# Kernel tuning notes

Hardware: AMD Instinct MI355X
Metric: run time of the kernel (lower is better)

The kernel has to match this reference:

```python
import jax, jax.numpy as jnp
import numpy as np

HEADS = 16


def _linear(x, w, b):
    # torch nn.Linear: y = x @ W^T + b, W: (out, in)
    return jnp.einsum('bld,od->blo', x, w) + b


def setup_inputs() -> dict:
    key = jax.random.key(0)
    ks = jax.random.split(key, 11)
    B, L, QD, KVD = 8, 2048, 1024, 1024
    s_in = 1.0 / np.sqrt(QD)
    return {
        'query': jax.random.normal(ks[0], (B, L, QD), jnp.float32),
        'key':   jax.random.normal(ks[1], (B, L, KVD), jnp.float32),
        'value': jax.random.normal(ks[2], (B, L, KVD), jnp.float32),
        'wq_w': jax.random.normal(ks[3], (KVD, QD), jnp.float32) * s_in,
        'wq_b': jnp.zeros((KVD,), jnp.float32),
        'wk_w': jax.random.normal(ks[4], (KVD, KVD), jnp.float32) * s_in,
        'wk_b': jnp.zeros((KVD,), jnp.float32),
        'wv_w': jax.random.normal(ks[5], (KVD, KVD), jnp.float32) * s_in,
        'wv_b': jnp.zeros((KVD,), jnp.float32),
        'fo_w': jax.random.normal(ks[6], (QD, KVD), jnp.float32) * s_in,
        'fo_b': jnp.zeros((QD,), jnp.float32),
    }


def reference(query, key, value, wq_w, wq_b, wk_w, wk_b, wv_w, wv_b, fo_w, fo_b):
    B, Lq, _ = query.shape
    Lk = key.shape[1]
    kvd = wq_w.shape[0]
    head_dim = kvd // HEADS
    # reshape WITHOUT transpose, exactly as the torch source: (B, L, heads, head_dim)
    q = _linear(query, wq_w, wq_b).reshape(B, Lq, HEADS, head_dim)
    k = _linear(key,   wk_w, wk_b).reshape(B, Lk, HEADS, head_dim)
    v = _linear(value, wv_w, wv_b).reshape(B, Lk, HEADS, head_dim)
    scale = 1.0 / jnp.sqrt(jnp.float32(head_dim))
    # Faithful to source: seq axis acts as 'h'; heads axis is contracted (i,j).
    scores = jnp.einsum('bhid,bhjd->bhij', q, k) * scale  # (B, L, heads, heads)
    weights = jax.nn.softmax(scores, axis=-1)
    out = jnp.einsum('bhij,bhjd->bhid', weights, v)       # (B, L, heads, head_dim)
    out = out.reshape(B, Lq, kvd)
    return _linear(out, fo_w, fo_b)
```

## Files before the change

### kernel.cpp

```cpp
#include <hip/hip_runtime.h>
#include <hip/hip_bf16.h>


typedef __attribute__((ext_vector_type(8))) __bf16 bf16x8;
typedef __attribute__((ext_vector_type(4))) float f32x4;

#define BM 128
#define BN 128
#define BK 64

__device__ __forceinline__ float bf2f(ushort u) {
  union { unsigned int i; float f; } c; c.i = ((unsigned int)u) << 16; return c.f;
}
__device__ __forceinline__ ushort f2b(float f) {
  union { float f; unsigned int i; } c; c.f = f;
  unsigned int x = c.i;
  return (ushort)((x + 0x7FFFu + ((x >> 16) & 1u)) >> 16);
}

__global__ __launch_bounds__(256)
void cvt_f32_bf16(const float* __restrict__ s, ushort* __restrict__ d, int n8)
{
  int i = blockIdx.x * 256 + threadIdx.x;
  if (i >= n8) return;
  const float4* sp = reinterpret_cast<const float4*>(s) + (size_t)i * 2;
  float4 a = sp[0], b = sp[1];
  ushort u[8] = { f2b(a.x), f2b(a.y), f2b(a.z), f2b(a.w),
                  f2b(b.x), f2b(b.y), f2b(b.z), f2b(b.w) };
  reinterpret_cast<uint4*>(d)[i] = *reinterpret_cast<uint4*>(u);
}

__global__ __launch_bounds__(256)
void cvt_wo_perm(const float* __restrict__ w, ushort* __restrict__ o)
{
  int t = blockIdx.x * 256 + threadIdx.x;
  int n  = t >> 7;
  int i8 = (t & 127) << 3;
  int blk = i8 >> 8, g = (i8 >> 6) & 3, i = (i8 >> 2) & 15;
  const float* src = w + (size_t)n * 1024;
  int c = blk * 16 + g * 4;
  float4 a = *reinterpret_cast<const float4*>(src + i * 64 + c);
  float4 b = *reinterpret_cast<const float4*>(src + (i + 1) * 64 + c);
  ushort u[8] = { f2b(a.x), f2b(a.y), f2b(a.z), f2b(a.w),
                  f2b(b.x), f2b(b.y), f2b(b.z), f2b(b.w) };
  *reinterpret_cast<uint4*>(o + (size_t)n * 1024 + i8) = *reinterpret_cast<uint4*>(u);
}

template<int CMODE>
__global__ __launch_bounds__(512, 2)
void gemm8p(const ushort* __restrict__ A, const ushort* __restrict__ Bw,
            const float* __restrict__ bias, void* __restrict__ Cv,
            int M, int N, int K)
{
  extern __shared__ ushort lds[];

  const int tid  = threadIdx.x;
  const int lane = tid & 63;
  const int wid  = tid >> 6;
  const int wm   = wid >> 2;
  const int wn   = wid & 3;

  const int nwg = gridDim.x * gridDim.y;
  int fid = blockIdx.y * gridDim.x + blockIdx.x;
  if ((nwg & 7) == 0) fid = (fid & 7) * (nwg >> 3) + (fid >> 3);
  const int bx = fid % gridDim.x;
  const int by = fid / gridDim.x;
  const int m0 = by * 256, n0 = bx * 256;

  const int NT = K >> 6;

  const int csw = ((lane & 7) ^ (lane >> 3)) << 3;
  auto STAGE = [&](int h, int kt, int b) {
    const ushort* base = (h >= 2) ? Bw : A;
    const int o0 = (h >= 2) ? n0 : m0;
    const int rl = (h & 1) * 128;
    #pragma unroll
    for (int j = 0; j < 2; ++j) {
      int rt = rl + j * 64 + wid * 8;
      const ushort* src = base + (size_t)(o0 + rt + (lane >> 3)) * K + kt * 64 + csw;
      ushort* dst = lds + b * 32768 + (h >= 2 ? 16384 : 0) + rt * 64;
      __builtin_amdgcn_global_load_lds(
          (const __attribute__((address_space(1))) void*)src,
          (__attribute__((address_space(3))) void*)dst, 16, 0, 0);
    }
  };

  auto LDA = [&](int b, int mi, int kk) -> bf16x8 {
    int row  = (mi & 3) * 16 + wm * 64 + (mi >> 2) * 128 + (lane & 15);
    int slot = kk * 4 + (lane >> 4);
    int byte = row * 128 + (((slot ^ (row & 7)) & 7) << 4);
    return *reinterpret_cast<const bf16x8*>((const char*)(lds + b * 32768) + byte);
  };
  auto LDB = [&](int b, int ni, int kk) -> bf16x8 {
    int row  = (ni & 1) * 16 + wn * 32 + (ni >> 1) * 128 + (lane & 15);
    int slot = kk * 4 + (lane >> 4);
    int byte = row * 128 + (((slot ^ (row & 7)) & 7) << 4);
    return *reinterpret_cast<const bf16x8*>((const char*)(lds + b * 32768 + 16384) + byte);
  };

  f32x4 acc[8][4] = {};
  bf16x8 af[4][2], bf[4][2];

  STAGE(0, 0, 0); STAGE(2, 0, 0); STAGE(3, 0, 0); STAGE(1, 0, 0);
  asm volatile("s_waitcnt vmcnt(4)" ::: "memory");
  __builtin_amdgcn_s_barrier();

  for (int t = 0; t < NT; ++t) {
    const int cur = t & 1;
    const int nxt = cur ^ 1;
    const bool pf = (t + 1) < NT;

    #pragma unroll
    for (int i = 0; i < 4; ++i) { af[i][0] = LDA(cur, i, 0); af[i][1] = LDA(cur, i, 1); }
    #pragma unroll
    for (int n = 0; n < 2; ++n) { bf[n][0] = LDB(cur, n, 0); bf[n][1] = LDB(cur, n, 1); }
    if (pf) { STAGE(0, t + 1, nxt); asm volatile("s_waitcnt vmcnt(4)" ::: "memory"); }
    else    {                       asm volatile("s_waitcnt vmcnt(2)" ::: "memory"); }
    __builtin_amdgcn_s_barrier();
    asm volatile("s_waitcnt lgkmcnt(0)" ::: "memory");
    __builtin_amdgcn_sched_barrier(0);
    __builtin_amdgcn_s_setprio(1);
    #pragma unroll
    for (int i = 0; i < 4; ++i)
      #pragma unroll
      for (int n = 0; n < 2; ++n)
        #pragma unroll
        for (int kk = 0; kk < 2; ++kk)
          acc[i][n] = __builtin_amdgcn_mfma_f32_16x16x32_bf16(af[i][kk], bf[n][kk], acc[i][n], 0, 0, 0);
    __builtin_amdgcn_s_setprio(0);
    __builtin_amdgcn_s_barrier();

    #pragma unroll
    for (int n = 0; n < 2; ++n) { bf[2 + n][0] = LDB(cur, 2 + n, 0); bf[2 + n][1] = LDB(cur, 2 + n, 1); }
    if (pf) { STAGE(2, t + 1, nxt); asm volatile("s_waitcnt vmcnt(4)" ::: "memory"); }
    else    {                       asm volatile("s_waitcnt vmcnt(0)" ::: "memory"); }
    __builtin_amdgcn_s_barrier();
    asm volatile("s_waitcnt lgkmcnt(0)" ::: "memory");
    __builtin_amdgcn_sched_barrier(0);
    __builtin_amdgcn_s_setprio(1);
    #pragma unroll
    for (int i = 0; i < 4; ++i)
      #pragma unroll
      for (int n = 0; n < 2; ++n)
        #pragma unroll
        for (int kk = 0; kk < 2; ++kk)
          acc[i][2 + n] = __builtin_amdgcn_mfma_f32_16x16x32_bf16(af[i][kk], bf[2 + n][kk], acc[i][2 + n], 0, 0, 0);
    __builtin_amdgcn_s_setprio(0);
    __builtin_amdgcn_s_barrier();

    #pragma unroll
    for (int i = 0; i < 4; ++i) { af[i][0] = LDA(cur, 4 + i, 0); af[i][1] = LDA(cur, 4 + i, 1); }
    if (pf) STAGE(3, t + 1, nxt);
    __builtin_amdgcn_s_barrier();
    asm volatile("s_waitcnt lgkmcnt(0)" ::: "memory");
    __builtin_amdgcn_sched_barrier(0);
    __builtin_amdgcn_s_setprio(1);
    #pragma unroll
    for (int i = 0; i < 4; ++i)
      #pragma unroll
      for (int n = 0; n < 2; ++n)
        #pragma unroll
        for (int kk = 0; kk < 2; ++kk)
          acc[4 + i][n] = __builtin_amdgcn_mfma_f32_16x16x32_bf16(af[i][kk], bf[n][kk], acc[4 + i][n], 0, 0, 0);
    __builtin_amdgcn_s_setprio(0);
    __builtin_amdgcn_s_barrier();

    if (pf) { STAGE(1, t + 1, nxt); asm volatile("s_waitcnt vmcnt(4)" ::: "memory"); }
    __builtin_amdgcn_s_barrier();
    __builtin_amdgcn_s_setprio(1);
    #pragma unroll
    for (int i = 0; i < 4; ++i)
      #pragma unroll
      for (int n = 0; n < 2; ++n)
        #pragma unroll
        for (int kk = 0; kk < 2; ++kk)
          acc[4 + i][2 + n] = __builtin_amdgcn_mfma_f32_16x16x32_bf16(af[i][kk], bf[2 + n][kk], acc[4 + i][2 + n], 0, 0, 0);
    __builtin_amdgcn_s_setprio(0);
    __builtin_amdgcn_s_barrier();
  }

  #pragma unroll
  for (int ni = 0; ni < 4; ++ni) {
    int col = n0 + (ni & 1) * 16 + wn * 32 + (ni >> 1) * 128 + (lane & 15);
    float bv = bias[col];
    #pragma unroll
    for (int mi = 0; mi < 8; ++mi) {
      int row0 = m0 + (mi & 3) * 16 + wm * 64 + (mi >> 2) * 128 + ((lane >> 4) << 2);
      #pragma unroll
      for (int q = 0; q < 4; ++q) {
        float v = acc[mi][ni][q] + bv;
        if constexpr (CMODE == 0)
          ((float*)Cv)[(size_t)(row0 + q) * N + col] = v;
        else if constexpr (CMODE == 1)
          ((ushort*)Cv)[(size_t)(row0 + q) * N + col] = f2b(v);
        else
          ((ushort*)Cv)[(size_t)(row0 + q) * N + ((col & 63) << 4) + (col >> 6)] = f2b(v);
      }
    }
  }
}

__global__ __launch_bounds__(256)
void attn_mfma(const ushort* __restrict__ Q, const ushort* __restrict__ Kh,
               const ushort* __restrict__ Vt, ushort* __restrict__ Ot, int P)
{
  const int lane = threadIdx.x & 63;
  const int wid  = threadIdx.x >> 6;
  const int g = lane >> 4, c = lane & 15;
  const int stride = gridDim.x * 4;

  for (int p = blockIdx.x * 4 + wid; p < P; p += stride) {
    const ushort* qb = Q  + (size_t)p * 1024;
    const ushort* kb = Kh + (size_t)p * 1024;
    const ushort* vb = Vt + (size_t)p * 1024;

    bf16x8 qf0 = *reinterpret_cast<const bf16x8*>(qb + c * 64 + g * 8);
    bf16x8 qf1 = *reinterpret_cast<const bf16x8*>(qb + c * 64 + 32 + g * 8);
    bf16x8 kf0 = *reinterpret_cast<const bf16x8*>(kb + c * 64 + g * 8);
    bf16x8 kf1 = *reinterpret_cast<const bf16x8*>(kb + c * 64 + 32 + g * 8);

    f32x4 s = {};
    s = __builtin_amdgcn_mfma_f32_16x16x32_bf16(kf0, qf0, s, 0, 0, 0);
    s = __builtin_amdgcn_mfma_f32_16x16x32_bf16(kf1, qf1, s, 0, 0, 0);

    float s0 = s[0] * 0.125f, s1 = s[1] * 0.125f;
    float s2 = s[2] * 0.125f, s3 = s[3] * 0.125f;
    float m = fmaxf(fmaxf(s0, s1), fmaxf(s2, s3));
    m = fmaxf(m, __shfl_xor(m, 16));
    m = fmaxf(m, __shfl_xor(m, 32));
    float e0 = __expf(s0 - m), e1 = __expf(s1 - m);
    float e2 = __expf(s2 - m), e3 = __expf(s3 - m);
    float sum = e0 + e1 + e2 + e3;
    sum += __shfl_xor(sum, 16);
    sum += __shfl_xor(sum, 32);
    float r = 1.0f / sum;

    uint pk0 = (uint)f2b(e0 * r) | ((uint)f2b(e1 * r) << 16);
    uint pk1 = (uint)f2b(e2 * r) | ((uint)f2b(e3 * r) << 16);
    int src = ((g & 1) << 5) | c;
    uint y0 = (uint)__shfl((int)pk0, src);
    uint y1 = (uint)__shfl((int)pk1, src);
    uint y2 = (uint)__shfl((int)pk0, src | 16);
    uint y3 = (uint)__shfl((int)pk1, src | 16);
    if (g >= 2) { y0 = 0; y1 = 0; y2 = 0; y3 = 0; }
    union { uint u[4]; bf16x8 v; } yu;
    yu.u[0] = y0; yu.u[1] = y1; yu.u[2] = y2; yu.u[3] = y3;

    ushort* ob = Ot + (size_t)p * 1024;
    #pragma unroll
    for (int blk = 0; blk < 4; ++blk) {
      bf16x8 vf = {};
      if (g < 2)
        vf = *reinterpret_cast<const bf16x8*>(vb + blk * 256 + c * 16 + g * 8);
      f32x4 o = {};
      o = __builtin_amdgcn_mfma_f32_16x16x32_bf16(vf, yu.v, o, 0, 0, 0);
      uint lo = (uint)f2b(o[0]) | ((uint)f2b(o[1]) << 16);
      uint hi = (uint)f2b(o[2]) | ((uint)f2b(o[3]) << 16);
      uint2 w2; w2.x = lo; w2.y = hi;
      *reinterpret_cast<uint2*>(ob + blk * 256 + g * 64 + c * 4) = w2;
    }
  }
}

template<bool A_IS_BF16, bool OUT_BF16>
__global__ __launch_bounds__(256)
void gemm_bt(const void* __restrict__ Av, const float* __restrict__ B,
             const float* __restrict__ bias, void* __restrict__ Cv,
             int M, int N, int K)
{
  __shared__ ushort As[BM * BK];
  __shared__ ushort Bs[BN * BK];

  const int tid  = threadIdx.x;
  const int lane = tid & 63;
  const int wid  = tid >> 6;
  const int wr   = wid >> 1;
  const int wc   = wid & 1;
  const int m0   = blockIdx.y * BM;
  const int n0   = blockIdx.x * BN;

  f32x4 acc[4][4] = {};

  const int r   = tid >> 1;
  const int seg = (tid & 1) * 32;

  for (int k0 = 0; k0 < K; k0 += BK) {
    {
      ushort tmp[32];
      if constexpr (A_IS_BF16) {
        const ushort* gA = (const ushort*)Av + (size_t)(m0 + r) * K + k0 + seg;
        #pragma unroll
        for (int u = 0; u < 4; ++u)
          *reinterpret_cast<uint4*>(&tmp[u * 8]) =
              *reinterpret_cast<const uint4*>(gA + u * 8);
      } else {
        const float* gA = (const float*)Av + (size_t)(m0 + r) * K + k0 + seg;
        #pragma unroll
        for (int u = 0; u < 8; ++u) {
          float4 f = *reinterpret_cast<const float4*>(gA + u * 4);
          tmp[u * 4 + 0] = f2b(f.x); tmp[u * 4 + 1] = f2b(f.y);
          tmp[u * 4 + 2] = f2b(f.z); tmp[u * 4 + 3] = f2b(f.w);
        }
      }
      #pragma unroll
      for (int s4 = 0; s4 < 4; ++s4) {
        int slot = (seg >> 3) + s4;
        int byte = r * 128 + ((slot ^ (r & 7)) << 4);
        *reinterpret_cast<uint4*>((char*)As + byte) =
            *reinterpret_cast<uint4*>(&tmp[s4 * 8]);
      }
    }
    {
      const float* gB = B + (size_t)(n0 + r) * K + k0 + seg;
      ushort tmp[32];
      #pragma unroll
      for (int u = 0; u < 8; ++u) {
        float4 f = *reinterpret_cast<const float4*>(gB + u * 4);
        tmp[u * 4 + 0] = f2b(f.x); tmp[u * 4 + 1] = f2b(f.y);
        tmp[u * 4 + 2] = f2b(f.z); tmp[u * 4 + 3] = f2b(f.w);
      }
      #pragma unroll
      for (int s4 = 0; s4 < 4; ++s4) {
        int slot = (seg >> 3) + s4;
        int byte = r * 128 + ((slot ^ (r & 7)) << 4);
        *reinterpret_cast<uint4*>((char*)Bs + byte) =
            *reinterpret_cast<uint4*>(&tmp[s4 * 8]);
      }
    }
    __syncthreads();

    #pragma unroll
    for (int kk = 0; kk < 2; ++kk) {
      const int kbase = kk * 32 + ((lane >> 4) << 3);
      const int slot  = kbase >> 3;
      bf16x8 af[4], bfr[4];
      #pragma unroll
      for (int mi = 0; mi < 4; ++mi) {
        int row = wr * 64 + mi * 16 + (lane & 15);
        af[mi] = *reinterpret_cast<const bf16x8*>(
            (const char*)As + row * 128 + ((slot ^ (row & 7)) << 4));
      }
      #pragma unroll
      for (int ni = 0; ni < 4; ++ni) {
        int row = wc * 64 + ni * 16 + (lane & 15);
        bfr[ni] = *reinterpret_cast<const bf16x8*>(
            (const char*)Bs + row * 128 + ((slot ^ (row & 7)) << 4));
      }
      #pragma unroll
      for (int mi = 0; mi < 4; ++mi)
        #pragma unroll
        for (int ni = 0; ni < 4; ++ni)
          acc[mi][ni] = __builtin_amdgcn_mfma_f32_16x16x32_bf16(
              af[mi], bfr[ni], acc[mi][ni], 0, 0, 0);
    }
    __syncthreads();
  }

  #pragma unroll
  for (int ni = 0; ni < 4; ++ni) {
    int col = n0 + wc * 64 + ni * 16 + (lane & 15);
    float bv = bias[col];
    #pragma unroll
    for (int mi = 0; mi < 4; ++mi) {
      int row0 = m0 + wr * 64 + mi * 16 + ((lane >> 4) << 2);
      #pragma unroll
      for (int q = 0; q < 4; ++q) {
        float v = acc[mi][ni][q] + bv;
        if constexpr (OUT_BF16)
          ((ushort*)Cv)[(size_t)(row0 + q) * N + col] = f2b(v);
        else
          ((float*)Cv)[(size_t)(row0 + q) * N + col] = v;
      }
    }
  }
}

__global__ __launch_bounds__(256)
void attn_kernel(const ushort* __restrict__ Q, const ushort* __restrict__ Kh,
                 const ushort* __restrict__ V, ushort* __restrict__ O)
{
  __shared__ float smem[4][3][16][68];
  const int tid  = threadIdx.x;
  const int wid  = tid >> 6;
  const int lane = tid & 63;
  const size_t p = (size_t)blockIdx.x * 4 + wid;

  {
    const ushort* srcs[3] = { Q + p * 1024, Kh + p * 1024, V + p * 1024 };
    const int i  = lane >> 2;
    const int d0 = (lane & 3) * 16;
    #pragma unroll
    for (int m = 0; m < 3; ++m) {
      const ushort* s = srcs[m] + lane * 16;
      ushort u[16];
      *reinterpret_cast<uint4*>(&u[0]) = *reinterpret_cast<const uint4*>(s);
      *reinterpret_cast<uint4*>(&u[8]) = *reinterpret_cast<const uint4*>(s + 8);
      #pragma unroll
      for (int e = 0; e < 16; ++e) smem[wid][m][i][d0 + e] = bf2f(u[e]);
    }
  }
  __syncthreads();

  const int i  = lane >> 2;
  const int jg = lane & 3;
  const float* qrow = smem[wid][0][i];
  const float* k0r = smem[wid][1][jg * 4 + 0];
  const float* k1r = smem[wid][1][jg * 4 + 1];
  const float* k2r = smem[wid][1][jg * 4 + 2];
  const float* k3r = smem[wid][1][jg * 4 + 3];

  float s0 = 0.f, s1 = 0.f, s2 = 0.f, s3 = 0.f;
  #pragma unroll
  for (int d = 0; d < 64; ++d) {
    float qv = qrow[d];
    s0 += qv * k0r[d]; s1 += qv * k1r[d];
    s2 += qv * k2r[d]; s3 += qv * k3r[d];
  }
  const float scale = 0.125f;
  s0 *= scale; s1 *= scale; s2 *= scale; s3 *= scale;

  float mx = fmaxf(fmaxf(s0, s1), fmaxf(s2, s3));
  mx = fmaxf(mx, __shfl_xor(mx, 1));
  mx = fmaxf(mx, __shfl_xor(mx, 2));
  float e0 = __expf(s0 - mx), e1 = __expf(s1 - mx);
  float e2 = __expf(s2 - mx), e3 = __expf(s3 - mx);
  float sum = e0 + e1 + e2 + e3;
  sum += __shfl_xor(sum, 1);
  sum += __shfl_xor(sum, 2);
  float inv = 1.0f / sum;
  e0 *= inv; e1 *= inv; e2 *= inv; e3 *= inv;

  const float* v0r = smem[wid][2][jg * 4 + 0];
  const float* v1r = smem[wid][2][jg * 4 + 1];
  const float* v2r = smem[wid][2][jg * 4 + 2];
  const float* v3r = smem[wid][2][jg * 4 + 3];
  ushort* orow = O + p * 1024 + i * 64;

  #pragma unroll
  for (int cc = 0; cc < 4; ++cc) {
    float po[16];
    #pragma unroll
    for (int dd = 0; dd < 16; ++dd) {
      int d = cc * 16 + dd;
      po[dd] = e0 * v0r[d] + e1 * v1r[d] + e2 * v2r[d] + e3 * v3r[d];
    }
    #pragma unroll
    for (int dd = 0; dd < 16; ++dd) {
      po[dd] += __shfl_xor(po[dd], 1);
      po[dd] += __shfl_xor(po[dd], 2);
    }
    if (jg == cc) {
      #pragma unroll
      for (int dd = 0; dd < 16; ++dd) orow[cc * 16 + dd] = f2b(po[dd]);
    }
  }
}

extern "C" void kernel_launch(void* const* d_in, const int* in_sizes, int n_in,
                              void* d_out, int out_size, void* d_ws, size_t ws_size,
                              hipStream_t stream)
{
  const float* query = (const float*)d_in[0];
  const float* key_  = (const float*)d_in[1];
  const float* value = (const float*)d_in[2];
  const float* wq_w  = (const float*)d_in[3];
  const float* wq_b  = (const float*)d_in[4];
  const float* wk_w  = (const float*)d_in[5];
  const float* wk_b  = (const float*)d_in[6];
  const float* wv_w  = (const float*)d_in[7];
  const float* wv_b  = (const float*)d_in[8];
  const float* fo_w  = (const float*)d_in[9];
  const float* fo_b  = (const float*)d_in[10];

  const int K = 1024, N = 1024;
  const int M = in_sizes[0] / K;
  const size_t slot = (size_t)M * N;
  const size_t wsl  = (size_t)N * K;
  const size_t need = (4 * slot + 4 * wsl) * sizeof(ushort);

  if (ws_size >= need && (M % 256) == 0 && N == 1024 && K == 1024) {
    hipFuncSetAttribute(reinterpret_cast<const void*>(gemm8p<0>),
                        hipFuncAttributeMaxDynamicSharedMemorySize, 131072);
    hipFuncSetAttribute(reinterpret_cast<const void*>(gemm8p<1>),
                        hipFuncAttributeMaxDynamicSharedMemorySize, 131072);
    hipFuncSetAttribute(reinterpret_cast<const void*>(gemm8p<2>),
                        hipFuncAttributeMaxDynamicSharedMemorySize, 131072);

    ushort* S0 = (ushort*)d_ws;
    ushort* S1 = S0 + slot;
    ushort* S2 = S1 + slot;
    ushort* S3 = S2 + slot;
    ushort* Wq = S3 + slot;
    ushort* Wk = Wq + wsl;
    ushort* Wv = Wk + wsl;
    ushort* Wo = Wv + wsl;

    const int n8w = (int)(wsl / 8);
    const int n8s = (int)(slot / 8);
    dim3 g8(N / 256, M / 256);
    dim3 b8(512);

    cvt_f32_bf16<<<dim3((n8w + 255) / 256), dim3(256), 0, stream>>>(wq_w, Wq, n8w);
    cvt_f32_bf16<<<dim3((n8w + 255) / 256), dim3(256), 0, stream>>>(wk_w, Wk, n8w);
    cvt_f32_bf16<<<dim3((n8w + 255) / 256), dim3(256), 0, stream>>>(wv_w, Wv, n8w);
    cvt_wo_perm <<<dim3(512), dim3(256), 0, stream>>>(fo_w, Wo);

    cvt_f32_bf16<<<dim3((n8s + 255) / 256), dim3(256), 0, stream>>>(query, S0, n8s);
    gemm8p<1><<<g8, b8, 131072, stream>>>(S0, Wq, wq_b, S1, M, N, K);
    cvt_f32_bf16<<<dim3((n8s + 255) / 256), dim3(256), 0, stream>>>(key_, S0, n8s);
    gemm8p<1><<<g8, b8, 131072, stream>>>(S0, Wk, wk_b, S2, M, N, K);
    cvt_f32_bf16<<<dim3((n8s + 255) / 256), dim3(256), 0, stream>>>(value, S0, n8s);
    gemm8p<2><<<g8, b8, 131072, stream>>>(S0, Wv, wv_b, S3, M, N, K);

    attn_mfma<<<dim3(2048), dim3(256), 0, stream>>>(S1, S2, S3, S0, M);
    gemm8p<0><<<g8, b8, 131072, stream>>>(S0, Wo, fo_b, d_out, M, N, K);
  } else {
    dim3 grid(N / BN, M / BM);
    ushort* Qb = (ushort*)d_ws;
    ushort* Kb = Qb + slot;
    ushort* Vb = Kb + slot;
    ushort* Ob = Vb + slot;
    gemm_bt<false, true><<<grid, dim3(256), 0, stream>>>(query, wq_w, wq_b, Qb, M, N, K);
    gemm_bt<false, true><<<grid, dim3(256), 0, stream>>>(key_,  wk_w, wk_b, Kb, M, N, K);
    gemm_bt<false, true><<<grid, dim3(256), 0, stream>>>(value, wv_w, wv_b, Vb, M, N, K);
    attn_kernel<<<dim3(M / 4), dim3(256), 0, stream>>>(Qb, Kb, Vb, Ob);
    gemm_bt<true, false><<<grid, dim3(256), 0, stream>>>(Ob, fo_w, fo_b, d_out, M, N, K);
  }
}
```

Baseline: 279.6 us.

## Fuse fp32-to-bf16 activation conversion into GEMM A-tile loading

The Q/K/V projection GEMMs now read fp32 activations directly, converting them to bf16 in registers and writing the swizzled tile into LDS, which removes three separate conversion kernels and their round trips of bf16 activation copies through memory. The three weight conversions are merged into one launch. Launch bounds drop from two waves-per-SIMD target to one, giving more registers for the extra fp32 staging buffers but possibly lowering occupancy. The A path moves from async global-to-LDS loads to register loads plus explicit LDS writes, which adds VGPR pressure and waitcnt scheduling risk.

```diff
diff --git a/kernel.cpp b/kernel.cpp
--- a/kernel.cpp
+++ b/kernel.cpp
@@ -19,15 +19,20 @@
 }
 
 __global__ __launch_bounds__(256)
-void cvt_f32_bf16(const float* __restrict__ s, ushort* __restrict__ d, int n8)
+void cvt_w3(const float* __restrict__ a, const float* __restrict__ b,
+            const float* __restrict__ c, ushort* __restrict__ dst, int n8each)
 {
   int i = blockIdx.x * 256 + threadIdx.x;
-  if (i >= n8) return;
-  const float4* sp = reinterpret_cast<const float4*>(s) + (size_t)i * 2;
-  float4 a = sp[0], b = sp[1];
-  ushort u[8] = { f2b(a.x), f2b(a.y), f2b(a.z), f2b(a.w),
-                  f2b(b.x), f2b(b.y), f2b(b.z), f2b(b.w) };
-  reinterpret_cast<uint4*>(d)[i] = *reinterpret_cast<uint4*>(u);
+  if (i >= 3 * n8each) return;
+  const float* s; int j;
+  if (i < n8each)            { s = a; j = i; }
+  else if (i < 2 * n8each)   { s = b; j = i - n8each; }
+  else                       { s = c; j = i - 2 * n8each; }
+  const float4* sp = reinterpret_cast<const float4*>(s) + (size_t)j * 2;
+  float4 x = sp[0], y = sp[1];
+  ushort u[8] = { f2b(x.x), f2b(x.y), f2b(x.z), f2b(x.w),
+                  f2b(y.x), f2b(y.y), f2b(y.z), f2b(y.w) };
+  reinterpret_cast<uint4*>(dst)[i] = *reinterpret_cast<uint4*>(u);
 }
 
 __global__ __launch_bounds__(256)
@@ -46,9 +51,9 @@
   *reinterpret_cast<uint4*>(o + (size_t)n * 1024 + i8) = *reinterpret_cast<uint4*>(u);
 }
 
-template<int CMODE>
-__global__ __launch_bounds__(512, 2)
-void gemm8p(const ushort* __restrict__ A, const ushort* __restrict__ Bw,
+template<int AMODE, int CMODE>
+__global__ __launch_bounds__(512, 1)
+void gemm8p(const void* __restrict__ Av, const ushort* __restrict__ Bw,
             const float* __restrict__ bias, void* __restrict__ Cv,
             int M, int N, int K)
 {
@@ -70,18 +75,53 @@
   const int NT = K >> 6;
 
   const int csw = ((lane & 7) ^ (lane >> 3)) << 3;
-  auto STAGE = [&](int h, int kt, int b) {
-    const ushort* base = (h >= 2) ? Bw : A;
-    const int o0 = (h >= 2) ? n0 : m0;
-    const int rl = (h & 1) * 128;
+
+  auto STAGE_B = [&](int h, int kt, int b) {
     #pragma unroll
     for (int j = 0; j < 2; ++j) {
-      int rt = rl + j * 64 + wid * 8;
-      const ushort* src = base + (size_t)(o0 + rt + (lane >> 3)) * K + kt * 64 + csw;
-      ushort* dst = lds + b * 32768 + (h >= 2 ? 16384 : 0) + rt * 64;
+      int rt = h * 128 + j * 64 + wid * 8;
+      const ushort* src = Bw + (size_t)(n0 + rt + (lane >> 3)) * K + kt * 64 + csw;
+      ushort* dst = lds + b * 32768 + 16384 + rt * 64;
       __builtin_amdgcn_global_load_lds(
           (const __attribute__((address_space(1))) void*)src,
           (__attribute__((address_space(3))) void*)dst, 16, 0, 0);
+    }
+  };
+  auto STAGE_A16 = [&](int h, int kt, int b) {
+    const ushort* A16 = (const ushort*)Av;
+    #pragma unroll
+    for (int j = 0; j < 2; ++j) {
+      int rt = h * 128 + j * 64 + wid * 8;
+      const ushort* src = A16 + (size_t)(m0 + rt + (lane >> 3)) * K + kt * 64 + csw;
+      ushort* dst = lds + b * 32768 + rt * 64;
+      __builtin_amdgcn_global_load_lds(
+          (const __attribute__((address_space(1))) void*)src,
+          (__attribute__((address_space(3))) void*)dst, 16, 0, 0);
+    }
+  };
+
+  float4 areg[8];
+  auto A_ISSUE = [&](int kt) {
+    const float* Af = (const float*)Av;
+    #pragma unroll
+    for (int u = 0; u < 4; ++u) {
+      int r = u * 64 + wid * 8 + (lane >> 3);
+      int s = (lane & 7) ^ (r & 7);
+      const float* src = Af + (size_t)(m0 + r) * K + kt * 64 + s * 8;
+      areg[2 * u]     = *reinterpret_cast<const float4*>(src);
+      areg[2 * u + 1] = *reinterpret_cast<const float4*>(src + 4);
+    }
+  };
+  auto A_WRITE = [&](int b) {
+    #pragma unroll
+    for (int u = 0; u < 4; ++u) {
+      int r = u * 64 + wid * 8 + (lane >> 3);
+      ushort tmp[8] = { f2b(areg[2*u].x),   f2b(areg[2*u].y),
+                        f2b(areg[2*u].z),   f2b(areg[2*u].w),
+                        f2b(areg[2*u+1].x), f2b(areg[2*u+1].y),
+                        f2b(areg[2*u+1].z), f2b(areg[2*u+1].w) };
+      *reinterpret_cast<uint4*>(&lds[b * 32768 + r * 64 + (lane & 7) * 8]) =
+          *reinterpret_cast<uint4*>(tmp);
     }
   };
 
@@ -101,8 +141,15 @@
   f32x4 acc[8][4] = {};
   bf16x8 af[4][2], bf[4][2];
 
-  STAGE(0, 0, 0); STAGE(2, 0, 0); STAGE(3, 0, 0); STAGE(1, 0, 0);
-  asm volatile("s_waitcnt vmcnt(4)" ::: "memory");
+  if constexpr (AMODE == 0) {
+    A_ISSUE(0); STAGE_B(0, 0, 0); STAGE_B(1, 0, 0);
+    asm volatile("s_waitcnt vmcnt(0)" ::: "memory");
+    A_WRITE(0);
+    asm volatile("s_waitcnt lgkmcnt(0)" ::: "memory");
+  } else {
+    STAGE_A16(0, 0, 0); STAGE_B(0, 0, 0); STAGE_B(1, 0, 0); STAGE_A16(1, 0, 0);
+    asm volatile("s_waitcnt vmcnt(4)" ::: "memory");
+  }
   __builtin_amdgcn_s_barrier();
 
   for (int t = 0; t < NT; ++t) {
@@ -114,8 +161,15 @@
     for (int i = 0; i < 4; ++i) { af[i][0] = LDA(cur, i, 0); af[i][1] = LDA(cur, i, 1); }
     #pragma unroll
     for (int n = 0; n < 2; ++n) { bf[n][0] = LDB(cur, n, 0); bf[n][1] = LDB(cur, n, 1); }
-    if (pf) { STAGE(0, t + 1, nxt); asm volatile("s_waitcnt vmcnt(4)" ::: "memory"); }
-    else    {                       asm volatile("s_waitcnt vmcnt(2)" ::: "memory"); }
+    if constexpr (AMODE == 0) {
+      if (pf) { A_ISSUE(t + 1); STAGE_B(0, t + 1, nxt);
+                asm volatile("s_waitcnt vmcnt(10)" ::: "memory"); }
+      else    { asm volatile("s_waitcnt vmcnt(0)"  ::: "memory"); }
+    } else {
+      if (pf) { STAGE_A16(0, t + 1, nxt);
+                asm volatile("s_waitcnt vmcnt(4)" ::: "memory"); }
+      else    { asm volatile("s_waitcnt vmcnt(2)" ::: "memory"); }
+    }
     __builtin_amdgcn_s_barrier();
     asm volatile("s_waitcnt lgkmcnt(0)" ::: "memory");
     __builtin_amdgcn_sched_barrier(0);
@@ -132,8 +186,13 @@
 
     #pragma unroll
     for (int n = 0; n < 2; ++n) { bf[2 + n][0] = LDB(cur, 2 + n, 0); bf[2 + n][1] = LDB(cur, 2 + n, 1); }
-    if (pf) { STAGE(2, t + 1, nxt); asm volatile("s_waitcnt vmcnt(4)" ::: "memory"); }
-    else    {                       asm volatile("s_waitcnt vmcnt(0)" ::: "memory"); }
+    if constexpr (AMODE == 0) {
+      if (pf) STAGE_B(1, t + 1, nxt);
+    } else {
+      if (pf) { STAGE_B(0, t + 1, nxt);
+                asm volatile("s_waitcnt vmcnt(4)" ::: "memory"); }
+      else    { asm volatile("s_waitcnt vmcnt(0)" ::: "memory"); }
+    }
     __builtin_amdgcn_s_barrier();
     asm volatile("s_waitcnt lgkmcnt(0)" ::: "memory");
     __builtin_amdgcn_sched_barrier(0);
@@ -150,7 +209,12 @@
 
     #pragma unroll
     for (int i = 0; i < 4; ++i) { af[i][0] = LDA(cur, 4 + i, 0); af[i][1] = LDA(cur, 4 + i, 1); }
-    if (pf) STAGE(3, t + 1, nxt);
+    if constexpr (AMODE == 0) {
+      if (pf) { asm volatile("s_waitcnt vmcnt(2)" ::: "memory");
+                A_WRITE(nxt); }
+    } else {
+      if (pf) STAGE_B(1, t + 1, nxt);
+    }
     __builtin_amdgcn_s_barrier();
     asm volatile("s_waitcnt lgkmcnt(0)" ::: "memory");
     __builtin_amdgcn_sched_barrier(0);
@@ -165,7 +229,10 @@
     __builtin_amdgcn_s_setprio(0);
     __builtin_amdgcn_s_barrier();
 
-    if (pf) { STAGE(1, t + 1, nxt); asm volatile("s_waitcnt vmcnt(4)" ::: "memory"); }
+    if constexpr (AMODE == 1) {
+      if (pf) { STAGE_A16(1, t + 1, nxt);
+                asm volatile("s_waitcnt vmcnt(4)" ::: "memory"); }
+    }
     __builtin_amdgcn_s_barrier();
     __builtin_amdgcn_s_setprio(1);
     #pragma unroll
@@ -479,11 +546,11 @@
   const size_t need = (4 * slot + 4 * wsl) * sizeof(ushort);
 
   if (ws_size >= need && (M % 256) == 0 && N == 1024 && K == 1024) {
-    hipFuncSetAttribute(reinterpret_cast<const void*>(gemm8p<0>),
+    hipFuncSetAttribute(reinterpret_cast<const void*>(gemm8p<0, 1>),
                         hipFuncAttributeMaxDynamicSharedMemorySize, 131072);
-    hipFuncSetAttribute(reinterpret_cast<const void*>(gemm8p<1>),
+    hipFuncSetAttribute(reinterpret_cast<const void*>(gemm8p<0, 2>),
                         hipFuncAttributeMaxDynamicSharedMemorySize, 131072);
-    hipFuncSetAttribute(reinterpret_cast<const void*>(gemm8p<2>),
+    hipFuncSetAttribute(reinterpret_cast<const void*>(gemm8p<1, 0>),
                         hipFuncAttributeMaxDynamicSharedMemorySize, 131072);
 
     ushort* S0 = (ushort*)d_ws;
@@ -491,29 +558,22 @@
     ushort* S2 = S1 + slot;
     ushort* S3 = S2 + slot;
     ushort* Wq = S3 + slot;
-    ushort* Wk = Wq + wsl;
-    ushort* Wv = Wk + wsl;
-    ushort* Wo = Wv + wsl;
+    ushort* Wo = Wq + 3 * wsl;
 
     const int n8w = (int)(wsl / 8);
-    const int n8s = (int)(slot / 8);
     dim3 g8(N / 256, M / 256);
     dim3 b8(512);
 
-    cvt_f32_bf16<<<dim3((n8w + 255) / 256), dim3(256), 0, stream>>>(wq_w, Wq, n8w);
-    cvt_f32_bf16<<<dim3((n8w + 255) / 256), dim3(256), 0, stream>>>(wk_w, Wk, n8w);
-    cvt_f32_bf16<<<dim3((n8w + 255) / 256), dim3(256), 0, stream>>>(wv_w, Wv, n8w);
-    cvt_wo_perm <<<dim3(512), dim3(256), 0, stream>>>(fo_w, Wo);
-
-    cvt_f32_bf16<<<dim3((n8s + 255) / 256), dim3(256), 0, stream>>>(query, S0, n8s);
-    gemm8p<1><<<g8, b8, 131072, stream>>>(S0, Wq, wq_b, S1, M, N, K);
-    cvt_f32_bf16<<<dim3((n8s + 255) / 256), dim3(256), 0, stream>>>(key_, S0, n8s);
-    gemm8p<1><<<g8, b8, 131072, stream>>>(S0, Wk, wk_b, S2, M, N, K);
-    cvt_f32_bf16<<<dim3((n8s + 255) / 256), dim3(256), 0, stream>>>(value, S0, n8s);
-    gemm8p<2><<<g8, b8, 131072, stream>>>(S0, Wv, wv_b, S3, M, N, K);
+    cvt_w3<<<dim3((3 * n8w + 255) / 256), dim3(256), 0, stream>>>(
+        wq_w, wk_w, wv_w, Wq, n8w);
+    cvt_wo_perm<<<dim3(512), dim3(256), 0, stream>>>(fo_w, Wo);
+
+    gemm8p<0, 1><<<g8, b8, 131072, stream>>>(query, Wq,           wq_b, S1, M, N, K);
+    gemm8p<0, 1><<<g8, b8, 131072, stream>>>(key_,  Wq + wsl,     wk_b, S2, M, N, K);
+    gemm8p<0, 2><<<g8, b8, 131072, stream>>>(value, Wq + 2 * wsl, wv_b, S3, M, N, K);
 
     attn_mfma<<<dim3(2048), dim3(256), 0, stream>>>(S1, S2, S3, S0, M);
-    gemm8p<0><<<g8, b8, 131072, stream>>>(S0, Wo, fo_b, d_out, M, N, K);
+    gemm8p<1, 0><<<g8, b8, 131072, stream>>>(S0, Wo, fo_b, d_out, M, N, K);
   } else {
     dim3 grid(N / BN, M / BM);
     ushort* Qb = (ushort*)d_ws;
```

Measured after the change: 322.2 us. +15.2%, slower.
